# Kernel optimization log

Measured on AMD Instinct MI355X. Metric: run time of the kernel, lower is better.

## Reference

```python
import jax, jax.numpy as jnp
import numpy as np

EPS = 1e-5
B, C, T = 128, 64, 1000          # batch, EEG channels, time samples
NCLU, HID, NOUT = 8, 512, 4      # clusters, head hidden dim, outputs (=feature_dim)


def _conv1d(x, w):
    # x: (N, Cin, T), w: (Cout, Cin, K), valid conv along time
    return jax.lax.conv_general_dilated(x, w, (1,), 'VALID',
                                        dimension_numbers=('NCH', 'OIH', 'NCH'))


def _bn(x, g, b, m, v):
    # eval-mode BatchNorm over channel dim of (N, C, T)
    return (x - m[None, :, None]) * (g / jnp.sqrt(v + EPS))[None, :, None] + b[None, :, None]


def _pool3(x):
    # maxpool kernel 3 stride 3 along time
    return jax.lax.reduce_window(x, -jnp.inf, jax.lax.max, (1, 1, 3), (1, 1, 3), 'VALID')


def setup_inputs() -> dict:
    key = jax.random.key(0)
    ks = jax.random.split(key, 12)
    def nrm(k, shape, fan):
        return jax.random.normal(k, shape, jnp.float32) / np.float32(np.sqrt(fan))
    inp = {
        'x': jax.random.normal(ks[0], (B, C, T), jnp.float32),
        'cluster_ids': jax.random.randint(ks[1], (B,), 0, NCLU, jnp.int32),
        # Deep4Net-style backbone params
        'w_time': nrm(ks[2], (25, 1, 10), 10),
        'b_time': jnp.zeros((25,), jnp.float32),
        'w_spat': nrm(ks[3], (25, 25, C), 25 * C),
        'w2': nrm(ks[4], (50, 25, 10), 250),
        'w3': nrm(ks[5], (100, 50, 10), 500),
        'w4': nrm(ks[6], (200, 100, 10), 1000),
        'w_cls': nrm(ks[7], (NOUT, 200, 7), 1400),
        'b_cls': jnp.zeros((NOUT,), jnp.float32),
        # per-cluster expert head params
        'hW1': nrm(ks[8], (NCLU, HID, NOUT), NOUT),
        'hb1': jnp.zeros((NCLU, HID), jnp.float32),
        'hW2': nrm(ks[9], (NCLU, NOUT, HID), HID),
        'hb2': jnp.zeros((NCLU, NOUT), jnp.float32),
        'hg': jnp.ones((NCLU, HID), jnp.float32),
        'hbe': jnp.zeros((NCLU, HID), jnp.float32),
        'hm': jnp.zeros((NCLU, HID), jnp.float32),
        'hv': jnp.ones((NCLU, HID), jnp.float32),
    }
    for i, c in zip((1, 2, 3, 4), (25, 50, 100, 200)):
        inp[f'g{i}'] = jnp.ones((c,), jnp.float32)
        inp[f'be{i}'] = jnp.zeros((c,), jnp.float32)
        inp[f'm{i}'] = jnp.zeros((c,), jnp.float32)
        inp[f'v{i}'] = jnp.ones((c,), jnp.float32)
    return inp


def reference(x, cluster_ids, w_time, b_time, w_spat, w2, w3, w4, w_cls, b_cls,
              hW1, hb1, hW2, hb2, hg, hbe, hm, hv,
              g1, be1, m1, v1, g2, be2, m2, v2, g3, be3, m3, v3, g4, be4, m4, v4):
    b_, c_, t_ = x.shape
    # conv_time: same 25 temporal filters applied per EEG channel -> (B, C, 25, T1)
    h = _conv1d(x.reshape(b_ * c_, 1, t_), w_time) + b_time[None, :, None]
    h = h.reshape(b_, c_, 25, -1)
    # conv_spat: collapse EEG channel axis -> (B, 25, T1)
    z = jnp.einsum('bcft,gfc->bgt', h, w_spat)
    z = _pool3(jax.nn.elu(_bn(z, g1, be1, m1, v1)))
    for w, g, be, m, v in ((w2, g2, be2, m2, v2), (w3, g3, be3, m3, v3), (w4, g4, be4, m4, v4)):
        z = _pool3(jax.nn.elu(_bn(_conv1d(z, w), g, be, m, v)))
    # final_conv_length='auto': classifier conv reduces time dim to 1 -> (B, NOUT)
    feats = (_conv1d(z, w_cls) + b_cls[None, :, None])[:, :, 0]
    # per-sample expert head routing (Linear -> BN(eval) -> ReLU -> [Dropout eval] -> Linear)
    h1 = jnp.einsum('bf,bhf->bh', feats, hW1[cluster_ids]) + hb1[cluster_ids]
    h1 = (h1 - hm[cluster_ids]) * (hg[cluster_ids] / jnp.sqrt(hv[cluster_ids] + EPS)) + hbe[cluster_ids]
    h1 = jax.nn.relu(h1)
    return jnp.einsum('bh,boh->bo', h1, hW2[cluster_ids]) + hb2[cluster_ids]
```

## Files before the change

### kernel.cpp

```cpp
#include <hip/hip_runtime.h>
#include <math.h>

#define EPS_BN 1e-5f

typedef __attribute__((ext_vector_type(8))) short short8;
typedef __attribute__((ext_vector_type(4))) float f32x4;

__device__ __forceinline__ unsigned short f2bf(float f) {
    unsigned int u = __float_as_uint(f);
    u = (u + 0x7fffu + ((u >> 16) & 1u)) >> 16;
    return (unsigned short)u;
}
__device__ __forceinline__ float bf2f(unsigned short s) {
    return __uint_as_float(((unsigned int)s) << 16);
}
__device__ __forceinline__ float elu1(float y) { return y > 0.f ? y : expm1f(y); }
__device__ __forceinline__ float warp_sum(float v) {
    for (int off = 32; off > 0; off >>= 1) v += __shfl_down(v, off);
    return v;
}

#define UW1 0
#define UW2 20480
#define UW3 40960
#define UW4 122880
#define BB1 0
#define BB2 32
#define BB3 96
#define BB4 224
#define UZ1 0
#define UZ2 1351680
#define UZ3 2228224
#define UZ4 2752512

__global__ __launch_bounds__(256) void kprep(
    const float* __restrict__ w_time, const float* __restrict__ b_time,
    const float* __restrict__ w_spat,
    const float* __restrict__ w2, const float* __restrict__ w3,
    const float* __restrict__ w4,
    const float* __restrict__ g1, const float* __restrict__ be1,
    const float* __restrict__ m1, const float* __restrict__ v1,
    const float* __restrict__ g2, const float* __restrict__ be2,
    const float* __restrict__ m2, const float* __restrict__ v2,
    const float* __restrict__ g3, const float* __restrict__ be3,
    const float* __restrict__ m3, const float* __restrict__ v3,
    const float* __restrict__ g4, const float* __restrict__ be4,
    const float* __restrict__ m4, const float* __restrict__ v4,
    unsigned short* __restrict__ wsu, float* __restrict__ biasf) {
    int idx = blockIdx.x * 256 + threadIdx.x;
    if (idx < 20480) {
        int k = idx >> 11, g = (idx >> 6) & 31, c = idx & 63;
        float val = 0.f;
        if (g < 25) {
            float s = 0.f;
#pragma unroll
            for (int f = 0; f < 25; ++f)
                s = fmaf(w_spat[g * 1600 + f * 64 + c], w_time[f * 10 + k], s);
            val = s * (g1[g] * rsqrtf(v1[g] + EPS_BN));
        }
        wsu[UW1 + idx] = f2bf(val);
    } else if (idx < 40960) {
        int j = idx - 20480;
        int k = j >> 11, g = (j >> 5) & 63, c = j & 31;
        float val = 0.f;
        if (g < 50 && c < 25)
            val = w2[(g * 25 + c) * 10 + k] * (g2[g] * rsqrtf(v2[g] + EPS_BN));
        wsu[UW2 + j] = f2bf(val);
    } else if (idx < 122880) {
        int j = idx - 40960;
        int k = j >> 13, g = (j >> 6) & 127, c = j & 63;
        float val = 0.f;
        if (g < 100 && c < 50)
            val = w3[(g * 50 + c) * 10 + k] * (g3[g] * rsqrtf(v3[g] + EPS_BN));
        wsu[UW3 + j] = f2bf(val);
    } else if (idx < 409600) {
        int j = idx - 122880;
        int k = j / 28672, r = j % 28672, g = r >> 7, c = r & 127;
        float val = 0.f;
        if (g < 200 && c < 100)
            val = w4[(g * 100 + c) * 10 + k] * (g4[g] * rsqrtf(v4[g] + EPS_BN));
        wsu[UW4 + j] = f2bf(val);
    } else if (idx < 410048) {
        int j = idx - 409600;
        if (j < 32) {
            int g = j; float val = 0.f;
            if (g < 25) {
                float beff = 0.f;
                for (int f = 0; f < 25; ++f) {
                    float a = 0.f;
                    for (int c = 0; c < 64; ++c) a += w_spat[g * 1600 + f * 64 + c];
                    beff = fmaf(a, b_time[f], beff);
                }
                float sc = g1[g] * rsqrtf(v1[g] + EPS_BN);
                val = be1[g] - m1[g] * sc + beff * sc;
            }
            biasf[BB1 + g] = val;
        } else if (j < 96) {
            int g = j - 32; float val = 0.f;
            if (g < 50) { float sc = g2[g] * rsqrtf(v2[g] + EPS_BN); val = be2[g] - m2[g] * sc; }
            biasf[BB2 + g] = val;
        } else if (j < 224) {
            int g = j - 96; float val = 0.f;
            if (g < 100) { float sc = g3[g] * rsqrtf(v3[g] + EPS_BN); val = be3[g] - m3[g] * sc; }
            biasf[BB3 + g] = val;
        } else {
            int g = j - 224; float val = 0.f;
            if (g < 200) { float sc = g4[g] * rsqrtf(v4[g] + EPS_BN); val = be4[g] - m4[g] * sc; }
            biasf[BB4 + g] = val;
        }
    }
}

template<int CPAD, int RS, int SP, int TT, int TPC, int NCHUNK, int JMAX,
         int NTCH, int NGB, int GPAD, int TIN, int TPOOL, int GSTORE, int NGV,
         int ROWS_AL, int WPB, int T0B, bool ST1>
__global__ __launch_bounds__(64 * WPB) void kconv(
    const float* __restrict__ x, const unsigned short* __restrict__ zin,
    const unsigned short* __restrict__ wpk, const float* __restrict__ bias,
    unsigned short* __restrict__ zout) {
    __shared__ __align__(16) unsigned short xT[ROWS_AL * RS];
    __shared__ __align__(16) unsigned short zb[WPB * TPC * 16 * 32];

    const int b = blockIdx.x, by = blockIdx.y;
    const int t = threadIdx.x;
    const int t0b = by * T0B;

    if constexpr (ST1) {
        const float* xb = x + b * 64000;
        for (int idx = t; idx < 32 * (ROWS_AL / 4); idx += 64 * WPB) {
            int cp = idx / (ROWS_AL / 4), t4 = idx % (ROWS_AL / 4);
            int r0 = t4 * 4, tg = t0b + r0;
            float4 va = {0, 0, 0, 0}, vb = {0, 0, 0, 0};
            if (tg < 1000) {
                va = *(const float4*)(xb + (2 * cp) * 1000 + tg);
                vb = *(const float4*)(xb + (2 * cp + 1) * 1000 + tg);
            }
            const float* pa = (const float*)&va;
            const float* pb = (const float*)&vb;
#pragma unroll
            for (int i2 = 0; i2 < 4; ++i2) {
                unsigned int pk = (unsigned int)f2bf(pa[i2]) |
                                  ((unsigned int)f2bf(pb[i2]) << 16);
                *(unsigned int*)&xT[(r0 + i2) * RS + 2 * cp] = pk;
            }
        }
    } else {
        const unsigned short* zi = zin + b * TIN * CPAD;
        for (int idx = t; idx < ROWS_AL * (CPAD / 2); idx += 64 * WPB) {
            int r = idx / (CPAD / 2), cp = idx % (CPAD / 2);
            unsigned int v = (r < TIN) ? *(const unsigned int*)&zi[r * CPAD + 2 * cp] : 0u;
            *(unsigned int*)&xT[r * RS + 2 * cp] = v;
        }
    }
    __syncthreads();

    const int lane = t & 63;
    const int wv = __builtin_amdgcn_readfirstlane(t >> 6);
    const int jobid = by * WPB + wv;
    const int gbi = jobid / NTCH, tci = jobid % NTCH;
    const bool active = (gbi < NGB);
    const int lm = lane & 15, h8 = lane >> 4;
    const int tl0 = tci * 96 - t0b;
    const int po0 = tci * 32;

    f32x4 acc[TT][2];
#pragma unroll
    for (int i = 0; i < TT; ++i) {
        acc[i][0] = (f32x4){0.f, 0.f, 0.f, 0.f};
        acc[i][1] = (f32x4){0.f, 0.f, 0.f, 0.f};
    }

    if (active) {
        const int abase = (tl0 + lm) * RS + h8 * 8;
        const unsigned short* wp = wpk + (gbi * 32 + lm) * CPAD + h8 * 8;
#pragma unroll
        for (int k = 0; k < 10; ++k) {
            short8 w0[SP], w1[SP];
#pragma unroll
            for (int s = 0; s < SP; ++s) {
                w0[s] = *(const short8*)(wp + k * (GPAD * CPAD) + s * 32);
                w1[s] = *(const short8*)(wp + k * (GPAD * CPAD) + 16 * CPAD + s * 32);
            }
#pragma unroll
            for (int s = 0; s < SP; ++s) {
#pragma unroll
                for (int tt = 0; tt < TT; ++tt) {
                    short8 a = *(const short8*)&xT[abase + (tt * 16 + k) * RS + s * 32];
                    acc[tt][0] = __builtin_amdgcn_mfma_f32_16x16x32_bf16(
                        a, w0[s], acc[tt][0], 0, 0, 0);
                    acc[tt][1] = __builtin_amdgcn_mfma_f32_16x16x32_bf16(
                        a, w1[s], acc[tt][1], 0, 0, 0);
                }
            }
        }

        float bv0 = bias[gbi * 32 + lm];
        float bv1 = bias[gbi * 32 + 16 + lm];
        unsigned short* zbw = &zb[wv * (TPC * 16 * 32)];
        const int gloc = lane & 31, hh = lane >> 5;
#pragma unroll
        for (int ch = 0; ch < NCHUNK; ++ch) {
#pragma unroll
            for (int ti = 0; ti < TPC; ++ti) {
                int ttg = ch * TPC + ti;
#pragma unroll
                for (int r = 0; r < 4; ++r) {
                    float v0 = elu1(acc[ttg][0][r] + bv0);
                    float v1 = elu1(acc[ttg][1][r] + bv1);
                    int row = ti * 16 + 4 * h8 + r;
                    zbw[row * 32 + lm] = f2bf(v0);
                    zbw[row * 32 + 16 + lm] = f2bf(v1);
                }
            }
#pragma unroll
            for (int j = 0; j < JMAX; ++j) {
                int po = hh + 2 * j;
                if (3 * po + 2 < TPC * 16) {
                    float q0 = bf2f(zbw[(3 * po) * 32 + gloc]);
                    float q1 = bf2f(zbw[(3 * po + 1) * 32 + gloc]);
                    float q2 = bf2f(zbw[(3 * po + 2) * 32 + gloc]);
                    float mx = fmaxf(q0, fmaxf(q1, q2));
                    int poa = po0 + ch * 16 + po;
                    int ga = gbi * 32 + gloc;
                    if (poa < TPOOL && ga < GSTORE)
                        zout[b * TPOOL * GSTORE + poa * GSTORE + ga] =
                            (ga < NGV) ? f2bf(mx) : (unsigned short)0;
                }
            }
        }
    }
}

__global__ __launch_bounds__(256) void k5(
    const unsigned short* __restrict__ z4, const float* __restrict__ w_cls,
    const float* __restrict__ b_cls, const int* __restrict__ cid,
    const float* __restrict__ hW1, const float* __restrict__ hb1,
    const float* __restrict__ hW2, const float* __restrict__ hb2,
    const float* __restrict__ hg, const float* __restrict__ hbe,
    const float* __restrict__ hm, const float* __restrict__ hv,
    float* __restrict__ out) {
    __shared__ float zs[1400];
    __shared__ float feats[4];
    __shared__ float h1s[512];
    const int b = blockIdx.x, t = threadIdx.x;
    for (int i = t; i < 1400; i += 256) zs[i] = bf2f(z4[b * 1400 + i]);
    __syncthreads();

    const int wv = t >> 6, lane = t & 63;
    {
        float p = 0.f;
        for (int i = lane; i < 1400; i += 64) {
            int po = i / 200, g = i - po * 200;
            p = fmaf(zs[i], w_cls[wv * 1400 + g * 7 + po], p);
        }
        p = warp_sum(p);
        if (lane == 0) feats[wv] = p + b_cls[wv];
    }
    __syncthreads();

    const int c = cid[b];
    const float f0 = feats[0], f1 = feats[1], f2 = feats[2], f3 = feats[3];
    for (int h = t; h < 512; h += 256) {
        const float* w1 = &hW1[(c * 512 + h) * 4];
        float v = f0 * w1[0] + f1 * w1[1] + f2 * w1[2] + f3 * w1[3] + hb1[c * 512 + h];
        float sc = hg[c * 512 + h] * rsqrtf(hv[c * 512 + h] + EPS_BN);
        v = (v - hm[c * 512 + h]) * sc + hbe[c * 512 + h];
        h1s[h] = fmaxf(v, 0.f);
    }
    __syncthreads();
    {
        float p = 0.f;
        for (int i = lane; i < 512; i += 64) p = fmaf(h1s[i], hW2[(c * 4 + wv) * 512 + i], p);
        p = warp_sum(p);
        if (lane == 0) out[b * 4 + wv] = p + hb2[c * 4 + wv];
    }
}

extern "C" void kernel_launch(void* const* d_in, const int* in_sizes, int n_in,
                              void* d_out, int out_size, void* d_ws, size_t ws_size,
                              hipStream_t stream) {
    const float* x      = (const float*)d_in[0];
    const int*   cid    = (const int*)d_in[1];
    const float* w_time = (const float*)d_in[2];
    const float* b_time = (const float*)d_in[3];
    const float* w_spat = (const float*)d_in[4];
    const float* w2     = (const float*)d_in[5];
    const float* w3     = (const float*)d_in[6];
    const float* w4     = (const float*)d_in[7];
    const float* w_cls  = (const float*)d_in[8];
    const float* b_cls  = (const float*)d_in[9];
    const float* hW1    = (const float*)d_in[10];
    const float* hb1    = (const float*)d_in[11];
    const float* hW2    = (const float*)d_in[12];
    const float* hb2    = (const float*)d_in[13];
    const float* hg     = (const float*)d_in[14];
    const float* hbe    = (const float*)d_in[15];
    const float* hm     = (const float*)d_in[16];
    const float* hv     = (const float*)d_in[17];
    const float* g1  = (const float*)d_in[18];
    const float* be1 = (const float*)d_in[19];
    const float* m1  = (const float*)d_in[20];
    const float* v1  = (const float*)d_in[21];
    const float* g2  = (const float*)d_in[22];
    const float* be2 = (const float*)d_in[23];
    const float* m2  = (const float*)d_in[24];
    const float* v2  = (const float*)d_in[25];
    const float* g3  = (const float*)d_in[26];
    const float* be3 = (const float*)d_in[27];
    const float* m3  = (const float*)d_in[28];
    const float* v3  = (const float*)d_in[29];
    const float* g4  = (const float*)d_in[30];
    const float* be4 = (const float*)d_in[31];
    const float* m4  = (const float*)d_in[32];
    const float* v4  = (const float*)d_in[33];

    unsigned short* wsu = (unsigned short*)d_ws;
    float* biasf = (float*)((char*)d_ws + 819200);
    unsigned short* zb = (unsigned short*)((char*)d_ws + 820992);
    float* out = (float*)d_out;

    kprep<<<1602, 256, 0, stream>>>(w_time, b_time, w_spat, w2, w3, w4,
                                    g1, be1, m1, v1, g2, be2, m2, v2,
                                    g3, be3, m3, v3, g4, be4, m4, v4,
                                    wsu, biasf);

    kconv<64, 72, 2, 6, 3, 2, 8, 11, 1, 32, 1000, 330, 32, 25, 204, 2, 192, true>
        <<<dim3(128, 6), 128, 0, stream>>>(x, nullptr, wsu + UW1, biasf + BB1, zb + UZ1);
    kconv<32, 40, 1, 6, 3, 2, 8, 4, 2, 64, 330, 107, 64, 50, 396, 4, 0, false>
        <<<dim3(128, 2), 256, 0, stream>>>(nullptr, zb + UZ1, wsu + UW2, biasf + BB2, zb + UZ2);
    kconv<64, 72, 2, 6, 3, 2, 8, 1, 4, 128, 107, 32, 128, 100, 108, 2, 0, false>
        <<<dim3(128, 2), 128, 0, stream>>>(nullptr, zb + UZ2, wsu + UW3, biasf + BB3, zb + UZ3);
    kconv<128, 136, 4, 2, 2, 1, 5, 1, 7, 224, 32, 7, 200, 200, 44, 2, 0, false>
        <<<dim3(128, 4), 128, 0, stream>>>(nullptr, zb + UZ3, wsu + UW4, biasf + BB4, zb + UZ4);

    k5<<<128, 256, 0, stream>>>(zb + UZ4, w_cls, b_cls, cid, hW1, hb1, hW2, hb2,
                                hg, hbe, hm, hv, out);
}
```

Before: 112.8 us.

## Fuse all conv stages and head into one per-sample megakernel in LDS

Replaces the four conv kernels and the head kernel with a single kernel, one block per sample, that keeps every intermediate activation in a large shared-memory buffer with aliased regions. Stage 1 is processed in two time passes to fit the input tile. This removes the global-memory round trips of intermediates and four kernel launches. The cost is parallelism: only 128 blocks of 4 waves with about 126KB of LDS each, so occupancy is one block per CU and there is less concurrency per stage than the previous multi-block grids.

```diff
diff --git a/kernel.cpp b/kernel.cpp
--- a/kernel.cpp
+++ b/kernel.cpp
@@ -28,10 +28,15 @@
 #define BB2 32
 #define BB3 96
 #define BB4 224
-#define UZ1 0
-#define UZ2 1351680
-#define UZ3 2228224
-#define UZ4 2752512
+
+#define L_XT   0
+#define L_Z2   0
+#define L_Z4   16384
+#define L_Z1   85248
+#define L_Z3   85248
+#define L_HEAD (85248 + 12288)
+#define L_ZB   116928
+#define XROWS  592
 
 __global__ __launch_bounds__(256) void kprep(
     const float* __restrict__ w_time, const float* __restrict__ b_time,
@@ -112,65 +117,31 @@
 }
 
 template<int CPAD, int RS, int SP, int TT, int TPC, int NCHUNK, int JMAX,
-         int NTCH, int NGB, int GPAD, int TIN, int TPOOL, int GSTORE, int NGV,
-         int ROWS_AL, int WPB, int T0B, bool ST1>
-__global__ __launch_bounds__(64 * WPB) void kconv(
-    const float* __restrict__ x, const unsigned short* __restrict__ zin,
-    const unsigned short* __restrict__ wpk, const float* __restrict__ bias,
-    unsigned short* __restrict__ zout) {
-    __shared__ __align__(16) unsigned short xT[ROWS_AL * RS];
-    __shared__ __align__(16) unsigned short zb[WPB * TPC * 16 * 32];
-
-    const int b = blockIdx.x, by = blockIdx.y;
-    const int t = threadIdx.x;
-    const int t0b = by * T0B;
-
-    if constexpr (ST1) {
-        const float* xb = x + b * 64000;
-        for (int idx = t; idx < 32 * (ROWS_AL / 4); idx += 64 * WPB) {
-            int cp = idx / (ROWS_AL / 4), t4 = idx % (ROWS_AL / 4);
-            int r0 = t4 * 4, tg = t0b + r0;
-            float4 va = {0, 0, 0, 0}, vb = {0, 0, 0, 0};
-            if (tg < 1000) {
-                va = *(const float4*)(xb + (2 * cp) * 1000 + tg);
-                vb = *(const float4*)(xb + (2 * cp + 1) * 1000 + tg);
-            }
-            const float* pa = (const float*)&va;
-            const float* pb = (const float*)&vb;
-#pragma unroll
-            for (int i2 = 0; i2 < 4; ++i2) {
-                unsigned int pk = (unsigned int)f2bf(pa[i2]) |
-                                  ((unsigned int)f2bf(pb[i2]) << 16);
-                *(unsigned int*)&xT[(r0 + i2) * RS + 2 * cp] = pk;
-            }
-        }
-    } else {
-        const unsigned short* zi = zin + b * TIN * CPAD;
-        for (int idx = t; idx < ROWS_AL * (CPAD / 2); idx += 64 * WPB) {
-            int r = idx / (CPAD / 2), cp = idx % (CPAD / 2);
-            unsigned int v = (r < TIN) ? *(const unsigned int*)&zi[r * CPAD + 2 * cp] : 0u;
-            *(unsigned int*)&xT[r * RS + 2 * cp] = v;
-        }
-    }
-    __syncthreads();
-
+         int NTCH, int GPAD, int TPOOL, int GSTORE, int NGV, int OUT_RS,
+         bool OUT_F32>
+__device__ __forceinline__ void conv_core(
+    const unsigned short* xT, const unsigned short* __restrict__ wpk,
+    const float* __restrict__ bias,
+    unsigned short* zout, float* zoutf, unsigned short* zb,
+    int t, int jbeg, int jend, int t0b) {
     const int lane = t & 63;
     const int wv = __builtin_amdgcn_readfirstlane(t >> 6);
-    const int jobid = by * WPB + wv;
-    const int gbi = jobid / NTCH, tci = jobid % NTCH;
-    const bool active = (gbi < NGB);
     const int lm = lane & 15, h8 = lane >> 4;
-    const int tl0 = tci * 96 - t0b;
-    const int po0 = tci * 32;
-
-    f32x4 acc[TT][2];
-#pragma unroll
-    for (int i = 0; i < TT; ++i) {
-        acc[i][0] = (f32x4){0.f, 0.f, 0.f, 0.f};
-        acc[i][1] = (f32x4){0.f, 0.f, 0.f, 0.f};
-    }
-
-    if (active) {
+    const int gloc = lane & 31, hh = lane >> 5;
+    unsigned short* zbw = zb + wv * (48 * 32);
+
+    for (int job = jbeg + wv; job < jend; job += 4) {
+        const int gbi = job / NTCH, tci = job % NTCH;
+        const int tl0 = tci * (TT * 16) - t0b;
+        const int po0 = tci * (NCHUNK * 16);
+
+        f32x4 acc[TT][2];
+#pragma unroll
+        for (int i = 0; i < TT; ++i) {
+            acc[i][0] = (f32x4){0.f, 0.f, 0.f, 0.f};
+            acc[i][1] = (f32x4){0.f, 0.f, 0.f, 0.f};
+        }
+
         const int abase = (tl0 + lm) * RS + h8 * 8;
         const unsigned short* wp = wpk + (gbi * 32 + lm) * CPAD + h8 * 8;
 #pragma unroll
@@ -194,10 +165,8 @@
             }
         }
 
-        float bv0 = bias[gbi * 32 + lm];
-        float bv1 = bias[gbi * 32 + 16 + lm];
-        unsigned short* zbw = &zb[wv * (TPC * 16 * 32)];
-        const int gloc = lane & 31, hh = lane >> 5;
+        const float bv0 = bias[gbi * 32 + lm];
+        const float bv1 = bias[gbi * 32 + 16 + lm];
 #pragma unroll
         for (int ch = 0; ch < NCHUNK; ++ch) {
 #pragma unroll
@@ -222,28 +191,85 @@
                     float mx = fmaxf(q0, fmaxf(q1, q2));
                     int poa = po0 + ch * 16 + po;
                     int ga = gbi * 32 + gloc;
-                    if (poa < TPOOL && ga < GSTORE)
-                        zout[b * TPOOL * GSTORE + poa * GSTORE + ga] =
-                            (ga < NGV) ? f2bf(mx) : (unsigned short)0;
+                    if (poa < TPOOL && ga < GSTORE) {
+                        if constexpr (OUT_F32)
+                            zoutf[poa * OUT_RS + ga] = mx;
+                        else
+                            zout[poa * OUT_RS + ga] =
+                                (ga < NGV) ? f2bf(mx) : (unsigned short)0;
+                    }
                 }
             }
         }
     }
 }
 
-__global__ __launch_bounds__(256) void k5(
-    const unsigned short* __restrict__ z4, const float* __restrict__ w_cls,
-    const float* __restrict__ b_cls, const int* __restrict__ cid,
+__global__ __launch_bounds__(256) void kmega(
+    const float* __restrict__ x, const unsigned short* __restrict__ wsu,
+    const float* __restrict__ biasf,
+    const float* __restrict__ w_cls, const float* __restrict__ b_cls,
+    const int* __restrict__ cid,
     const float* __restrict__ hW1, const float* __restrict__ hb1,
     const float* __restrict__ hW2, const float* __restrict__ hb2,
     const float* __restrict__ hg, const float* __restrict__ hbe,
     const float* __restrict__ hm, const float* __restrict__ hv,
     float* __restrict__ out) {
-    __shared__ float zs[1400];
-    __shared__ float feats[4];
-    __shared__ float h1s[512];
+    __shared__ __align__(16) unsigned char smem[129216];
+    unsigned short* xT  = (unsigned short*)(smem + L_XT);
+    unsigned short* z1u = (unsigned short*)(smem + L_Z1);
+    unsigned short* z2u = (unsigned short*)(smem + L_Z2);
+    unsigned short* z3u = (unsigned short*)(smem + L_Z3);
+    float*          z4f = (float*)(smem + L_Z4);
+    unsigned short* zb  = (unsigned short*)(smem + L_ZB);
+    float*          feats = (float*)(smem + L_HEAD);
+    float*          h1s   = (float*)(smem + L_HEAD + 16);
+
     const int b = blockIdx.x, t = threadIdx.x;
-    for (int i = t; i < 1400; i += 256) zs[i] = bf2f(z4[b * 1400 + i]);
+    const float* xb = x + b * 64000;
+
+#pragma unroll 1
+    for (int pass = 0; pass < 2; ++pass) {
+        const int t0 = pass * 576;
+        for (int idx = t; idx < 32 * (XROWS / 4); idx += 256) {
+            int cp = idx / (XROWS / 4), t4 = idx - cp * (XROWS / 4);
+            int r0 = 4 * t4, tg = t0 + r0;
+            float4 va = {0, 0, 0, 0}, vb = {0, 0, 0, 0};
+            if (tg < 1000) {
+                va = *(const float4*)(xb + (2 * cp) * 1000 + tg);
+                vb = *(const float4*)(xb + (2 * cp + 1) * 1000 + tg);
+            }
+            const float* pa = (const float*)&va;
+            const float* pb = (const float*)&vb;
+#pragma unroll
+            for (int i2 = 0; i2 < 4; ++i2) {
+                unsigned int pk = (unsigned int)f2bf(pa[i2]) |
+                                  ((unsigned int)f2bf(pb[i2]) << 16);
+                *(unsigned int*)&xT[(r0 + i2) * 72 + 2 * cp] = pk;
+            }
+        }
+        if (pass == 1) {
+            for (int i = t; i < 1320; i += 256)
+                *(unsigned int*)&z1u[330 * 40 + 2 * i] = 0u;
+        }
+        __syncthreads();
+        conv_core<64, 72, 2, 6, 3, 2, 8, 16, 32, 330, 32, 25, 40, false>(
+            xT, wsu + UW1, biasf + BB1, z1u, nullptr, zb, t,
+            pass == 0 ? 0 : 6, pass == 0 ? 6 : 11, t0);
+        __syncthreads();
+    }
+
+    conv_core<32, 40, 1, 6, 3, 2, 8, 4, 64, 107, 64, 50, 72, false>(
+        z1u, wsu + UW2, biasf + BB2, z2u, nullptr, zb, t, 0, 8, 0);
+    __syncthreads();
+
+    for (int i = t; i < 816; i += 256)
+        *(unsigned int*)&z3u[32 * 136 + 2 * i] = 0u;
+    conv_core<64, 72, 2, 6, 3, 2, 8, 1, 128, 32, 128, 100, 136, false>(
+        z2u, wsu + UW3, biasf + BB3, z3u, nullptr, zb, t, 0, 4, 0);
+    __syncthreads();
+
+    conv_core<128, 136, 4, 2, 2, 1, 4, 1, 224, 7, 200, 200, 200, true>(
+        z3u, wsu + UW4, biasf + BB4, nullptr, z4f, zb, t, 0, 7, 0);
     __syncthreads();
 
     const int wv = t >> 6, lane = t & 63;
@@ -251,7 +277,7 @@
         float p = 0.f;
         for (int i = lane; i < 1400; i += 64) {
             int po = i / 200, g = i - po * 200;
-            p = fmaf(zs[i], w_cls[wv * 1400 + g * 7 + po], p);
+            p = fmaf(z4f[i], w_cls[wv * 1400 + g * 7 + po], p);
         }
         p = warp_sum(p);
         if (lane == 0) feats[wv] = p + b_cls[wv];
@@ -270,7 +296,8 @@
     __syncthreads();
     {
         float p = 0.f;
-        for (int i = lane; i < 512; i += 64) p = fmaf(h1s[i], hW2[(c * 4 + wv) * 512 + i], p);
+        for (int i = lane; i < 512; i += 64)
+            p = fmaf(h1s[i], hW2[(c * 4 + wv) * 512 + i], p);
         p = warp_sum(p);
         if (lane == 0) out[b * 4 + wv] = p + hb2[c * 4 + wv];
     }
@@ -316,7 +343,6 @@
 
     unsigned short* wsu = (unsigned short*)d_ws;
     float* biasf = (float*)((char*)d_ws + 819200);
-    unsigned short* zb = (unsigned short*)((char*)d_ws + 820992);
     float* out = (float*)d_out;
 
     kprep<<<1602, 256, 0, stream>>>(w_time, b_time, w_spat, w2, w3, w4,
@@ -324,15 +350,6 @@
                                     g3, be3, m3, v3, g4, be4, m4, v4,
                                     wsu, biasf);
 
-    kconv<64, 72, 2, 6, 3, 2, 8, 11, 1, 32, 1000, 330, 32, 25, 204, 2, 192, true>
-        <<<dim3(128, 6), 128, 0, stream>>>(x, nullptr, wsu + UW1, biasf + BB1, zb + UZ1);
-    kconv<32, 40, 1, 6, 3, 2, 8, 4, 2, 64, 330, 107, 64, 50, 396, 4, 0, false>
-        <<<dim3(128, 2), 256, 0, stream>>>(nullptr, zb + UZ1, wsu + UW2, biasf + BB2, zb + UZ2);
-    kconv<64, 72, 2, 6, 3, 2, 8, 1, 4, 128, 107, 32, 128, 100, 108, 2, 0, false>
-        <<<dim3(128, 2), 128, 0, stream>>>(nullptr, zb + UZ2, wsu + UW3, biasf + BB3, zb + UZ3);
-    kconv<128, 136, 4, 2, 2, 1, 5, 1, 7, 224, 32, 7, 200, 200, 44, 2, 0, false>
-        <<<dim3(128, 4), 128, 0, stream>>>(nullptr, zb + UZ3, wsu + UW4, biasf + BB4, zb + UZ4);
-
-    k5<<<128, 256, 0, stream>>>(zb + UZ4, w_cls, b_cls, cid, hW1, hb1, hW2, hb2,
-                                hg, hbe, hm, hv, out);
-}
+    kmega<<<128, 256, 0, stream>>>(x, wsu, biasf, w_cls, b_cls, cid,
+                                   hW1, hb1, hW2, hb2, hg, hbe, hm, hv, out);
+}
```

Result: slower. 140.1 us (+24.2%).
